# Optimization experiments

Measured on AMD Instinct MI355X. Metric: run time of the kernel, lower is better.

## Reference

```python
import jax, jax.numpy as jnp
import numpy as np

B, T = 64, 1024
VOCAB, EMBED, HIDDEN = 55, 64, 128


def setup_inputs() -> dict:
    key = jax.random.key(0)
    ks = jax.random.split(key, 15)
    stdv = 1.0 / np.sqrt(HIDDEN)
    u = lambda k, s: jax.random.uniform(k, s, jnp.float32, -stdv, stdv)
    return {
        "x": jax.random.randint(ks[0], (B, T), 0, VOCAB),
        "emb": jax.random.normal(ks[1], (VOCAB, EMBED), jnp.float32),
        "w_ih0": u(ks[2], (HIDDEN, EMBED)),
        "b_ih0": u(ks[3], (HIDDEN,)),
        "w_hh0": u(ks[4], (HIDDEN, HIDDEN)),
        "b_hh0": u(ks[5], (HIDDEN,)),
        "w_ih1": u(ks[6], (HIDDEN, HIDDEN)),
        "b_ih1": u(ks[7], (HIDDEN,)),
        "w_hh1": u(ks[8], (HIDDEN, HIDDEN)),
        "b_hh1": u(ks[9], (HIDDEN,)),
        "attn_w": u(ks[10], (HIDDEN, HIDDEN)),
        "attn_b": u(ks[11], (HIDDEN,)),
        "fc_w": u(ks[12], (VOCAB, 2 * HIDDEN)),
        "fc_b": u(ks[13], (VOCAB,)),
    }


def reference(x, emb, w_ih0, b_ih0, w_hh0, b_hh0, w_ih1, b_ih1, w_hh1, b_hh1,
              attn_w, attn_b, fc_w, fc_b):
    Bx, Tx = x.shape
    H = w_hh0.shape[0]
    e = emb[x]  # [B, T, E]

    def step(carry, x_t):  # x_t: [B, E]
        h0, h1 = carry
        h0 = jnp.tanh(x_t @ w_ih0.T + b_ih0 + h0 @ w_hh0.T + b_hh0)
        h1 = jnp.tanh(h0 @ w_ih1.T + b_ih1 + h1 @ w_hh1.T + b_hh1)
        return (h0, h1), h1

    init = (jnp.zeros((Bx, H), e.dtype), jnp.zeros((Bx, H), e.dtype))
    _, outs = jax.lax.scan(step, init, jnp.swapaxes(e, 0, 1))  # [T, B, H]
    outs = jnp.swapaxes(outs, 0, 1)  # [B, T, H]

    Q = outs @ attn_w.T + attn_b  # [B, T, H]
    scores = jnp.einsum('bth,bsh->bts', Q, outs) / jnp.sqrt(jnp.asarray(H, e.dtype))
    causal = jnp.tril(jnp.ones((Tx, Tx), bool))  # [T, T]
    scores = jnp.where(causal[None], scores, jnp.asarray(-jnp.inf, scores.dtype))
    attn = jax.nn.softmax(scores, axis=-1)
    context = jnp.einsum('bts,bsh->bth', attn, outs)  # [B, T, H]

    combined = jnp.concatenate([outs, context], axis=-1)  # [B, T, 2H]
    logits = combined @ fc_w.T + fc_b  # [B, T, vocab]
    return logits
```

## Files before the change

### kernel.cpp

```cpp
#include <hip/hip_runtime.h>
#include <hip/hip_bf16.h>
#include <cstdint>
#include <cstddef>


typedef __attribute__((ext_vector_type(8))) short short8;
typedef __attribute__((ext_vector_type(4))) float f32x4;

__device__ __forceinline__ float bf2f(unsigned short u) {
    union { unsigned int i; float f; } c; c.i = ((unsigned int)u) << 16; return c.f;
}
__device__ __forceinline__ unsigned short f2bf(float f) {
    union { float f; unsigned int i; } c; c.f = f;
    unsigned int u = c.i;
    u += 0x7fffu + ((u >> 16) & 1u);
    return (unsigned short)(u >> 16);
}
__device__ __forceinline__ unsigned int pk_bf16(float lo, float hi) {
    union { __hip_bfloat162 h2; unsigned int u; } c;
    c.h2 = __float22bfloat162_rn(make_float2(lo, hi));
    return c.u;
}
__device__ __forceinline__ float fast_tanh(float x) {
    float e = __expf(2.0f * x);
    return 1.0f - 2.0f * __builtin_amdgcn_rcpf(e + 1.0f);
}
__device__ __forceinline__ void bar_lds() {
    asm volatile("s_waitcnt lgkmcnt(0)\n\ts_barrier" ::: "memory");
}
__device__ __forceinline__ short8 ld_a_bf16(const float* p) {
    const float4* q = (const float4*)p;
    float4 f0 = q[0], f1 = q[1];
    short8 r;
    r[0]=(short)f2bf(f0.x); r[1]=(short)f2bf(f0.y);
    r[2]=(short)f2bf(f0.z); r[3]=(short)f2bf(f0.w);
    r[4]=(short)f2bf(f1.x); r[5]=(short)f2bf(f1.y);
    r[6]=(short)f2bf(f1.z); r[7]=(short)f2bf(f1.w);
    return r;
}
__device__ __forceinline__ void ld_fc_hilo(const float* p, short8& hi, short8& lo) {
    const float4* q = (const float4*)p;
    float4 f0 = q[0], f1 = q[1];
    float ff[8] = {f0.x, f0.y, f0.z, f0.w, f1.x, f1.y, f1.z, f1.w};
#pragma unroll
    for (int i = 0; i < 8; ++i) {
        unsigned short hb = f2bf(ff[i]);
        hi[i] = (short)hb;
        lo[i] = (short)f2bf(ff[i] - bf2f(hb));
    }
}
__device__ __forceinline__ void rel_store(int* p, int v) {
    __threadfence();
    __hip_atomic_store(p, v, __ATOMIC_RELEASE, __HIP_MEMORY_SCOPE_AGENT);
}
__device__ __forceinline__ int rlx_load(const int* p) {
    return __hip_atomic_load(p, __ATOMIC_RELAXED, __HIP_MEMORY_SCOPE_AGENT);
}
__device__ __forceinline__ void acq_touch(const int* p) {
    (void)__hip_atomic_load(p, __ATOMIC_ACQUIRE, __HIP_MEMORY_SCOPE_AGENT);
}

__global__ __launch_bounds__(128)
void k_we(const float* __restrict__ emb, const float* __restrict__ w_ih0,
          const float* __restrict__ b_ih0, const float* __restrict__ b_hh0,
          float* __restrict__ WE)
{
    __shared__ float ev[64];
    const int i = threadIdx.x;
    const int v = blockIdx.x;
    if (i < 64) ev[i] = emb[v * 64 + i];
    __syncthreads();
    float s = b_ih0[i] + b_hh0[i];
    const float* wr = w_ih0 + i * 64;
#pragma unroll
    for (int k = 0; k < 64; ++k) s += wr[k] * ev[k];
    WE[v * 128 + i] = s;
}

__global__ __launch_bounds__(256)
void k_weg(const int* __restrict__ x, const float* __restrict__ WE,
           float* __restrict__ WEg)
{
    __shared__ int xv[32];
    const int tid = threadIdx.x;
    const int b   = blockIdx.y;
    const int t0  = blockIdx.x * 32;
    if (tid < 32) xv[tid] = x[b * 1024 + t0 + tid];
    __syncthreads();
#pragma unroll
    for (int it = 0; it < 4; ++it) {
        int tt = it * 8 + (tid >> 5);
        int c4 = tid & 31;
        float4 v = ((const float4*)(WE + xv[tt] * 128))[c4];
        ((float4*)(WEg + ((size_t)b * 1024 + t0 + tt) * 128))[c4] = v;
    }
}

__global__ __launch_bounds__(1024)
void k_zero(int* __restrict__ f)
{
    f[threadIdx.x] = 0;
}

__global__ __launch_bounds__(512, 1)
void k_fused(const float* __restrict__ WEg,
             const float* __restrict__ w_hh0,
             const float* __restrict__ w_ih1, const float* __restrict__ b_ih1,
             const float* __restrict__ w_hh1, const float* __restrict__ b_hh1,
             unsigned short* __restrict__ outs_bf,
             unsigned short* __restrict__ outsT,
             const float* __restrict__ attn_w, const float* __restrict__ attn_b,
             const float* __restrict__ fc_w, const float* __restrict__ fc_b,
             float* __restrict__ out, int* __restrict__ flags)
{
    __shared__ __align__(16) unsigned char smem[100352];
    __shared__ int sidx;
    const int bx   = blockIdx.x;
    const int tid  = threadIdx.x;
    const int w    = tid >> 6;
    const int lane = tid & 63;
    const int quad = lane >> 4;
    const int n    = lane & 15;

    if (bx < 4) {
        typedef unsigned short (*HBuf)[16][136];
        HBuf h0buf = (HBuf)(smem);
        HBuf h1buf = (HBuf)(smem + 8704);
        const int bbase = bx * 16;

        if (w < 4) {
            const int r0 = w * 32 + quad * 4;
            const int r1 = r0 + 16;
            short8 a0[2][4];
#pragma unroll
            for (int r = 0; r < 2; ++r) {
                const size_t mrow = (size_t)(w * 32 + r * 16 + n) * 128;
#pragma unroll
                for (int ks = 0; ks < 4; ++ks)
                    a0[r][ks] = ld_a_bf16(w_hh0 + mrow + ks * 32 + quad * 8);
            }
            const size_t wegB0 = (size_t)(bbase + n) * 131072 + r0;
            const size_t wegB1 = wegB0 + 16;
            {
                float4 p0 = *(const float4*)(WEg + wegB0);
                float4 p1 = *(const float4*)(WEg + wegB1);
                *(uint2*)&h0buf[0][n][r0] = make_uint2(
                    pk_bf16(fast_tanh(p0.x), fast_tanh(p0.y)),
                    pk_bf16(fast_tanh(p0.z), fast_tanh(p0.w)));
                *(uint2*)&h0buf[0][n][r1] = make_uint2(
                    pk_bf16(fast_tanh(p1.x), fast_tanh(p1.y)),
                    pk_bf16(fast_tanh(p1.z), fast_tanh(p1.w)));
            }
            float4 wA0 = *(const float4*)(WEg + wegB0 + 128);
            float4 wA1 = *(const float4*)(WEg + wegB1 + 128);
            float4 wB0 = *(const float4*)(WEg + wegB0 + 256);
            float4 wB1 = *(const float4*)(WEg + wegB1 + 256);
            float4 wC0 = *(const float4*)(WEg + wegB0 + 384);
            float4 wC1 = *(const float4*)(WEg + wegB1 + 384);
            __syncthreads();

            for (int t = 0; t < 1024; ++t) {
                const int p = t & 1;
                if (t < 1023) {
                    const unsigned short* h0p = &h0buf[p][n][quad * 8];
                    short8 bh[4];
#pragma unroll
                    for (int ks = 0; ks < 4; ++ks)
                        bh[ks] = *(const short8*)(h0p + ks * 32);
                    f32x4 c0 = (f32x4){wA0.x, wA0.y, wA0.z, wA0.w};
                    f32x4 c1 = (f32x4){wA1.x, wA1.y, wA1.z, wA1.w};
#pragma unroll
                    for (int ks = 0; ks < 4; ++ks) {
                        c0 = __builtin_amdgcn_mfma_f32_16x16x32_bf16(a0[0][ks], bh[ks], c0, 0,0,0);
                        c1 = __builtin_amdgcn_mfma_f32_16x16x32_bf16(a0[1][ks], bh[ks], c1, 0,0,0);
                    }
                    wA0 = wB0; wA1 = wB1; wB0 = wC0; wB1 = wC1;
                    const size_t tpre = (size_t)((t + 4 < 1024) ? t + 4 : 1023) * 128;
                    wC0 = *(const float4*)(WEg + wegB0 + tpre);
                    wC1 = *(const float4*)(WEg + wegB1 + tpre);
                    *(uint2*)&h0buf[p ^ 1][n][r0] = make_uint2(
                        pk_bf16(fast_tanh(c0[0]), fast_tanh(c0[1])),
                        pk_bf16(fast_tanh(c0[2]), fast_tanh(c0[3])));
                    *(uint2*)&h0buf[p ^ 1][n][r1] = make_uint2(
                        pk_bf16(fast_tanh(c1[0]), fast_tanh(c1[1])),
                        pk_bf16(fast_tanh(c1[2]), fast_tanh(c1[3])));
                }
                bar_lds();
                if ((t & 127) == 127) {
                    asm volatile("s_waitcnt vmcnt(0)" ::: "memory");
                    __syncthreads();
                    if (tid == 0) rel_store(flags + bx, t + 1);
                }
            }
        } else {
            const int w2 = w - 4;
            const int r0 = w2 * 32 + quad * 4;
            const int r1 = r0 + 16;
            short8 a1[2][4], a2[2][4];
#pragma unroll
            for (int r = 0; r < 2; ++r) {
                const size_t mrow = (size_t)(w2 * 32 + r * 16 + n) * 128;
#pragma unroll
                for (int ks = 0; ks < 4; ++ks) {
                    a1[r][ks] = ld_a_bf16(w_ih1 + mrow + ks * 32 + quad * 8);
                    a2[r][ks] = ld_a_bf16(w_hh1 + mrow + ks * 32 + quad * 8);
                }
            }
            f32x4 b1i[2];
#pragma unroll
            for (int r = 0; r < 2; ++r)
#pragma unroll
                for (int j = 0; j < 4; ++j) {
                    int row = w2 * 32 + r * 16 + quad * 4 + j;
                    b1i[r][j] = b_ih1[row] + b_hh1[row];
                }
            *(uint2*)&h1buf[0][n][r0] = make_uint2(0u, 0u);
            *(uint2*)&h1buf[0][n][r1] = make_uint2(0u, 0u);
            unsigned short* outp0 = outs_bf + (size_t)(bbase + n) * 131072 + r0;
            unsigned short* outp1 = outp0 + 16;
            __syncthreads();

            for (int t = 0; t < 1024; ++t) {
                const int p = t & 1;
                const unsigned short* h0p = &h0buf[p][n][quad * 8];
                const unsigned short* h1p = &h1buf[p][n][quad * 8];
                short8 bh0[4], bh1[4];
#pragma unroll
                for (int ks = 0; ks < 4; ++ks) {
                    bh0[ks] = *(const short8*)(h0p + ks * 32);
                    bh1[ks] = *(const short8*)(h1p + ks * 32);
                }
                f32x4 c0 = b1i[0], c1 = b1i[1];
                f32x4 d0 = (f32x4){0.f,0.f,0.f,0.f}, d1 = (f32x4){0.f,0.f,0.f,0.f};
#pragma unroll
                for (int ks = 0; ks < 4; ++ks) {
                    c0 = __builtin_amdgcn_mfma_f32_16x16x32_bf16(a1[0][ks], bh0[ks], c0, 0,0,0);
                    c1 = __builtin_amdgcn_mfma_f32_16x16x32_bf16(a1[1][ks], bh0[ks], c1, 0,0,0);
                    d0 = __builtin_amdgcn_mfma_f32_16x16x32_bf16(a2[0][ks], bh1[ks], d0, 0,0,0);
                    d1 = __builtin_amdgcn_mfma_f32_16x16x32_bf16(a2[1][ks], bh1[ks], d1, 0,0,0);
                }
                uint2 o0 = make_uint2(
                    pk_bf16(fast_tanh(c0[0] + d0[0]), fast_tanh(c0[1] + d0[1])),
                    pk_bf16(fast_tanh(c0[2] + d0[2]), fast_tanh(c0[3] + d0[3])));
                uint2 o1 = make_uint2(
                    pk_bf16(fast_tanh(c1[0] + d1[0]), fast_tanh(c1[1] + d1[1])),
                    pk_bf16(fast_tanh(c1[2] + d1[2]), fast_tanh(c1[3] + d1[3])));
                *(uint2*)&h1buf[p ^ 1][n][r0] = o0;
                *(uint2*)&h1buf[p ^ 1][n][r1] = o1;
                *(uint2*)(outp0 + (size_t)t * 128) = o0;
                *(uint2*)(outp1 + (size_t)t * 128) = o1;
                bar_lds();
                if ((t & 127) == 127) {
                    asm volatile("s_waitcnt vmcnt(0)" ::: "memory");
                    __syncthreads();
                    if (tid == 0) rel_store(flags + bx, t + 1);
                }
            }
        }
        return;
    }

    int* qcnt = flags + 768;
    const float cscale = 0.08838834764831845f;

    for (;;) {
        __syncthreads();
        if (tid == 0) sidx = atomicAdd(qcnt, 1);
        __syncthreads();
        const int idx = sidx;
        if (idx >= 1024) break;
        const int group = idx >> 6;
        const int b     = idx & 63;
        const int c     = group >> 1;

        if (!(group & 1)) {
            if (tid == 0) {
                while (rlx_load(flags + (b >> 4)) < (c + 1) * 128)
                    __builtin_amdgcn_s_sleep(100);
            }
            __syncthreads();
            acq_touch(flags + (b >> 4));

            typedef unsigned short (*LT)[130];
            LT lt = (LT)smem;
            const int t0 = c * 128;
            const unsigned int* src =
                (const unsigned int*)(outs_bf + ((size_t)b * 1024 + t0) * 128);
            for (int i2 = tid; i2 < 8192; i2 += 512) {
                int tr = i2 >> 6, h2 = i2 & 63;
                unsigned int v = src[tr * 64 + h2];
                lt[tr][h2 * 2]     = (unsigned short)(v & 0xffffu);
                lt[tr][h2 * 2 + 1] = (unsigned short)(v >> 16);
            }
            __syncthreads();
            unsigned int* dst = (unsigned int*)(outsT + (size_t)b * 131072);
            for (int i2 = tid; i2 < 8192; i2 += 512) {
                int h = i2 >> 6, t2 = i2 & 63;
                unsigned int v = (unsigned int)lt[t2 * 2][h] |
                                 ((unsigned int)lt[t2 * 2 + 1][h] << 16);
                dst[h * 512 + (t0 >> 1) + t2] = v;
            }
            asm volatile("s_waitcnt vmcnt(0)" ::: "memory");
            __syncthreads();
            if (tid == 0) rel_store(flags + 16 + b * 8 + c, 1);
            continue;
        }

        {
            const int qt = c;
            if (tid == 0) {
                for (int cc = 0; cc <= qt; ++cc)
                    while (rlx_load(flags + 16 + b * 8 + cc) < 1)
                        __builtin_amdgcn_s_sleep(100);
            }
            __syncthreads();
            acq_touch(flags + 16 + b * 8 + qt);

            unsigned short* lK = (unsigned short*)smem;
            unsigned short* lV = (unsigned short*)(smem + 32768);
            unsigned short* lP = (unsigned short*)(smem + 65536);
            unsigned short* lPw = lP + w * 2176;

            const unsigned short* outsB = outs_bf + (size_t)b * 131072;
            const int qrow = qt * 128 + w * 16 + n;

            short8 bo[4];
#pragma unroll
            for (int ks = 0; ks < 4; ++ks)
                bo[ks] = *(const short8*)(outsB + (size_t)qrow * 128 + ks * 32 + quad * 8);
#pragma unroll
            for (int mt = 0; mt < 8; ++mt) {
                short8 aw[4];
#pragma unroll
                for (int ks = 0; ks < 4; ++ks)
                    aw[ks] = ld_a_bf16(attn_w + (size_t)(mt * 16 + n) * 128 + ks * 32 + quad * 8);
                f32x4 cq;
#pragma unroll
                for (int r = 0; r < 4; ++r) cq[r] = attn_b[mt * 16 + quad * 4 + r];
#pragma unroll
                for (int ks = 0; ks < 4; ++ks)
                    cq = __builtin_amdgcn_mfma_f32_16x16x32_bf16(aw[ks], bo[ks], cq, 0,0,0);
                *(uint2*)&lPw[n * 136 + mt * 16 + quad * 4] =
                    make_uint2(pk_bf16(cq[0], cq[1]), pk_bf16(cq[2], cq[3]));
            }
            short8 qf[4];
#pragma unroll
            for (int ks = 0; ks < 4; ++ks)
                qf[ks] = *(const short8*)&lPw[n * 136 + ks * 32 + quad * 8];

            f32x4 accO[8];
#pragma unroll
            for (int dt = 0; dt < 8; ++dt) accO[dt] = (f32x4){0.f, 0.f, 0.f, 0.f};
            float mx = -1e30f, lsum = 0.f;

            for (int kt = 0; kt <= qt; ++kt) {
                __syncthreads();
                for (int cc = tid; cc < 2048; cc += 512) {
                    int row = cc >> 4, k8 = cc & 15;
                    uint4 vk = *(const uint4*)(outsB + (size_t)(kt * 128 + row) * 128 + k8 * 8);
                    *(uint4*)&lK[row * 128 + ((k8 ^ (row & 15)) << 3)] = vk;
                    uint4 vv = *(const uint4*)(outsT + ((size_t)b * 128 + row) * 1024 +
                                               kt * 128 + k8 * 8);
                    *(uint4*)&lV[row * 128 + ((k8 ^ (row & 15)) << 3)] = vv;
                }
                __syncthreads();
                f32x4 accS[8];
#pragma unroll
                for (int mt = 0; mt < 8; ++mt) {
                    short8 af[4];
#pragma unroll
                    for (int ks = 0; ks < 4; ++ks) {
                        int r = mt * 16 + n;
                        af[ks] = *(const short8*)&lK[r * 128 + (((ks * 4 + quad) ^ (r & 15)) << 3)];
                    }
                    f32x4 s = (f32x4){0.f, 0.f, 0.f, 0.f};
#pragma unroll
                    for (int ks = 0; ks < 4; ++ks)
                        s = __builtin_amdgcn_mfma_f32_16x16x32_bf16(af[ks], qf[ks], s, 0,0,0);
                    accS[mt] = s;
                }
                if (kt == qt) {
                    const int ql = w * 16 + n;
#pragma unroll
                    for (int mt = 0; mt < 8; ++mt)
#pragma unroll
                        for (int jv = 0; jv < 4; ++jv)
                            if (mt * 16 + quad * 4 + jv > ql) accS[mt][jv] = -1e30f;
                }
                float tmax = accS[0][0];
#pragma unroll
                for (int mt = 0; mt < 8; ++mt)
#pragma unroll
                    for (int jv = 0; jv < 4; ++jv) tmax = fmaxf(tmax, accS[mt][jv]);
                tmax = fmaxf(tmax, __shfl_xor(tmax, 16));
                tmax = fmaxf(tmax, __shfl_xor(tmax, 32));
                float nm = fmaxf(mx, tmax);
                float alpha = __expf((mx - nm) * cscale);
                float ss = 0.f;
#pragma unroll
                for (int mt = 0; mt < 8; ++mt)
#pragma unroll
                    for (int jv = 0; jv < 4; ++jv) {
                        float p = __expf((accS[mt][jv] - nm) * cscale);
                        accS[mt][jv] = p;
                        ss += p;
                    }
                ss += __shfl_xor(ss, 16);
                ss += __shfl_xor(ss, 32);
                lsum = lsum * alpha + ss;
                mx = nm;
#pragma unroll
                for (int mt = 0; mt < 8; ++mt)
                    *(uint2*)&lPw[n * 136 + mt * 16 + quad * 4] = make_uint2(
                        pk_bf16(accS[mt][0], accS[mt][1]),
                        pk_bf16(accS[mt][2], accS[mt][3]));
#pragma unroll
                for (int dt = 0; dt < 8; ++dt)
#pragma unroll
                    for (int jv = 0; jv < 4; ++jv) accO[dt][jv] *= alpha;
                short8 pf[4];
#pragma unroll
                for (int ks = 0; ks < 4; ++ks)
                    pf[ks] = *(const short8*)&lPw[n * 136 + ks * 32 + quad * 8];
#pragma unroll
                for (int dt = 0; dt < 8; ++dt) {
                    short8 vf[4];
#pragma unroll
                    for (int ks = 0; ks < 4; ++ks) {
                        int d = dt * 16 + n;
                        vf[ks] = *(const short8*)&lV[d * 128 + (((ks * 4 + quad) ^ (d & 15)) << 3)];
                    }
#pragma unroll
                    for (int ks = 0; ks < 4; ++ks)
                        accO[dt] = __builtin_amdgcn_mfma_f32_16x16x32_bf16(vf[ks], pf[ks], accO[dt], 0,0,0);
                }
            }
            {
                float inv = __builtin_amdgcn_rcpf(lsum);
#pragma unroll
                for (int dt = 0; dt < 8; ++dt)
                    *(uint2*)&lPw[n * 136 + dt * 16 + quad * 4] = make_uint2(
                        pk_bf16(accO[dt][0] * inv, accO[dt][1] * inv),
                        pk_bf16(accO[dt][2] * inv, accO[dt][3] * inv));
            }
            short8 bC[4];
#pragma unroll
            for (int ks = 0; ks < 4; ++ks)
                bC[ks] = *(const short8*)&lPw[n * 136 + ks * 32 + quad * 8];
#pragma unroll
            for (int mt = 0; mt < 4; ++mt) {
                const int vrow = mt * 16 + n;
                f32x4 acc;
#pragma unroll
                for (int r = 0; r < 4; ++r) {
                    int vv = mt * 16 + quad * 4 + r;
                    acc[r] = (vv < 55) ? fc_b[vv] : 0.f;
                }
#pragma unroll
                for (int cc = 0; cc < 8; ++cc) {
                    short8 hi, lo;
                    if (vrow < 55) {
                        ld_fc_hilo(fc_w + (size_t)vrow * 256 + cc * 32 + quad * 8, hi, lo);
                    } else {
#pragma unroll
                        for (int ii = 0; ii < 8; ++ii) { hi[ii] = 0; lo[ii] = 0; }
                    }
                    short8 bb = (cc < 4) ? bo[cc] : bC[cc - 4];
                    acc = __builtin_amdgcn_mfma_f32_16x16x32_bf16(hi, bb, acc, 0,0,0);
                    acc = __builtin_amdgcn_mfma_f32_16x16x32_bf16(lo, bb, acc, 0,0,0);
                }
#pragma unroll
                for (int r = 0; r < 4; ++r) {
                    int vv = mt * 16 + quad * 4 + r;
                    if (vv < 55)
                        out[((size_t)b * 1024 + qrow) * 55 + vv] = acc[r];
                }
            }
        }
    }
}

extern "C" void kernel_launch(void* const* d_in, const int* in_sizes, int n_in,
                              void* d_out, int out_size, void* d_ws, size_t ws_size,
                              hipStream_t stream)
{
    const int*   x      = (const int*)d_in[0];
    const float* emb    = (const float*)d_in[1];
    const float* w_ih0  = (const float*)d_in[2];
    const float* b_ih0  = (const float*)d_in[3];
    const float* w_hh0  = (const float*)d_in[4];
    const float* b_hh0  = (const float*)d_in[5];
    const float* w_ih1  = (const float*)d_in[6];
    const float* b_ih1  = (const float*)d_in[7];
    const float* w_hh1  = (const float*)d_in[8];
    const float* b_hh1  = (const float*)d_in[9];
    const float* attn_w = (const float*)d_in[10];
    const float* attn_b = (const float*)d_in[11];
    const float* fc_w   = (const float*)d_in[12];
    const float* fc_b   = (const float*)d_in[13];
    float* out = (float*)d_out;

    char* ws = (char*)d_ws;
    unsigned short* outs_bf = (unsigned short*)(ws);
    unsigned short* outsT   = (unsigned short*)(ws + ((size_t)16 << 20));
    float*          WEp     = (float*)         (ws + ((size_t)32 << 20));
    int*            flags   = (int*)           (ws + ((size_t)32 << 20) + (64 << 10));
    float*          WEg     = (float*)         (ws + ((size_t)33 << 20));

    k_zero<<<dim3(1), dim3(1024), 0, stream>>>(flags);
    k_we<<<dim3(55), dim3(128), 0, stream>>>(emb, w_ih0, b_ih0, b_hh0, WEp);
    k_weg<<<dim3(32, 64), dim3(256), 0, stream>>>(x, WEp, WEg);
    k_fused<<<dim3(256), dim3(512), 0, stream>>>(
        WEg, w_hh0, w_ih1, b_ih1, w_hh1, b_hh1, outs_bf, outsT,
        attn_w, attn_b, fc_w, fc_b, out, flags);
}
```

Before: 846.2 us.

## Fuse embedding precompute into persistent kernel and split tail attention tiles

Moves the word-embedding projection and gather into the persistent fused kernel as work items, with flags so the recurrent blocks start as soon as their batch rows are gathered. This removes two separate kernel launches. The last two query tiles, which have the longest causal spans, are split across several work items that write partial softmax state to a workspace and are merged afterwards, shortening the serial tail. The cost is extra flag spin-waits, partial-result traffic and more complex scheduling, which adds deadlock risk if the work-queue order is wrong.

Result: slower. 874.5 us (+3.3%).

```diff
diff --git a/kernel.cpp b/kernel.cpp
--- a/kernel.cpp
+++ b/kernel.cpp
@@ -27,6 +27,9 @@
 }
 __device__ __forceinline__ void bar_lds() {
     asm volatile("s_waitcnt lgkmcnt(0)\n\ts_barrier" ::: "memory");
+}
+__device__ __forceinline__ void drain_vm() {
+    asm volatile("s_waitcnt vmcnt(0)" ::: "memory");
 }
 __device__ __forceinline__ short8 ld_a_bf16(const float* p) {
     const float4* q = (const float4*)p;
@@ -60,50 +63,18 @@
     (void)__hip_atomic_load(p, __ATOMIC_ACQUIRE, __HIP_MEMORY_SCOPE_AGENT);
 }
 
-__global__ __launch_bounds__(128)
-void k_we(const float* __restrict__ emb, const float* __restrict__ w_ih0,
-          const float* __restrict__ b_ih0, const float* __restrict__ b_hh0,
-          float* __restrict__ WE)
-{
-    __shared__ float ev[64];
-    const int i = threadIdx.x;
-    const int v = blockIdx.x;
-    if (i < 64) ev[i] = emb[v * 64 + i];
-    __syncthreads();
-    float s = b_ih0[i] + b_hh0[i];
-    const float* wr = w_ih0 + i * 64;
-#pragma unroll
-    for (int k = 0; k < 64; ++k) s += wr[k] * ev[k];
-    WE[v * 128 + i] = s;
-}
-
-__global__ __launch_bounds__(256)
-void k_weg(const int* __restrict__ x, const float* __restrict__ WE,
-           float* __restrict__ WEg)
-{
-    __shared__ int xv[32];
-    const int tid = threadIdx.x;
-    const int b   = blockIdx.y;
-    const int t0  = blockIdx.x * 32;
-    if (tid < 32) xv[tid] = x[b * 1024 + t0 + tid];
-    __syncthreads();
-#pragma unroll
-    for (int it = 0; it < 4; ++it) {
-        int tt = it * 8 + (tid >> 5);
-        int c4 = tid & 31;
-        float4 v = ((const float4*)(WE + xv[tt] * 128))[c4];
-        ((float4*)(WEg + ((size_t)b * 1024 + t0 + tt) * 128))[c4] = v;
-    }
-}
-
 __global__ __launch_bounds__(1024)
 void k_zero(int* __restrict__ f)
 {
     f[threadIdx.x] = 0;
+    f[threadIdx.x + 1024] = 0;
 }
 
 __global__ __launch_bounds__(512, 1)
-void k_fused(const float* __restrict__ WEg,
+void k_fused(const int* __restrict__ x, const float* __restrict__ emb,
+             const float* __restrict__ w_ih0, const float* __restrict__ b_ih0,
+             const float* __restrict__ b_hh0,
+             float* __restrict__ WEp, float* __restrict__ WEg,
              const float* __restrict__ w_hh0,
              const float* __restrict__ w_ih1, const float* __restrict__ b_ih1,
              const float* __restrict__ w_hh1, const float* __restrict__ b_hh1,
@@ -111,6 +82,7 @@
              unsigned short* __restrict__ outsT,
              const float* __restrict__ attn_w, const float* __restrict__ attn_b,
              const float* __restrict__ fc_w, const float* __restrict__ fc_b,
+             float* __restrict__ part_ws,
              float* __restrict__ out, int* __restrict__ flags)
 {
     __shared__ __align__(16) unsigned char smem[100352];
@@ -127,6 +99,14 @@
         HBuf h0buf = (HBuf)(smem);
         HBuf h1buf = (HBuf)(smem + 8704);
         const int bbase = bx * 16;
+
+        if (tid == 0) {
+            for (int i = 0; i < 16; ++i)
+                while (rlx_load(flags + 16 + bbase + i) < 1)
+                    __builtin_amdgcn_s_sleep(16);
+            acq_touch(flags);
+        }
+        __syncthreads();
 
         if (w < 4) {
             const int r0 = w * 32 + quad * 4;
@@ -187,7 +167,7 @@
                 }
                 bar_lds();
                 if ((t & 127) == 127) {
-                    asm volatile("s_waitcnt vmcnt(0)" ::: "memory");
+                    drain_vm();
                     __syncthreads();
                     if (tid == 0) rel_store(flags + bx, t + 1);
                 }
@@ -251,7 +231,7 @@
                 *(uint2*)(outp1 + (size_t)t * 128) = o1;
                 bar_lds();
                 if ((t & 127) == 127) {
-                    asm volatile("s_waitcnt vmcnt(0)" ::: "memory");
+                    drain_vm();
                     __syncthreads();
                     if (tid == 0) rel_store(flags + bx, t + 1);
                 }
@@ -260,7 +240,22 @@
         return;
     }
 
-    int* qcnt = flags + 768;
+    if (bx == 4) {
+        for (int o = tid; o < 7040; o += 512) {
+            int v = o >> 7, i = o & 127;
+            float s = b_ih0[i] + b_hh0[i];
+            const float* wr = w_ih0 + i * 64;
+            const float* ev = emb + v * 64;
+#pragma unroll 8
+            for (int k = 0; k < 64; ++k) s += wr[k] * ev[k];
+            WEp[v * 128 + i] = s;
+        }
+        drain_vm();
+        __syncthreads();
+        if (tid == 0) rel_store(flags + 8, 1);
+    }
+
+    int* qcnt = flags + 1100;
     const float cscale = 0.08838834764831845f;
 
     for (;;) {
@@ -268,22 +263,60 @@
         if (tid == 0) sidx = atomicAdd(qcnt, 1);
         __syncthreads();
         const int idx = sidx;
-        if (idx >= 1024) break;
-        const int group = idx >> 6;
-        const int b     = idx & 63;
-        const int c     = group >> 1;
-
-        if (!(group & 1)) {
+        if (idx >= 1280) break;
+
+        if (idx < 64) {
+            const int b = idx;
             if (tid == 0) {
-                while (rlx_load(flags + (b >> 4)) < (c + 1) * 128)
-                    __builtin_amdgcn_s_sleep(100);
-            }
-            __syncthreads();
-            acq_touch(flags + (b >> 4));
-
+                while (rlx_load(flags + 8) < 1) __builtin_amdgcn_s_sleep(16);
+                acq_touch(flags + 8);
+            }
+            __syncthreads();
+            for (int t0 = 0; t0 < 1024; t0 += 16) {
+                int tt = t0 + (tid >> 5), c4 = tid & 31;
+                int xv = x[b * 1024 + tt];
+                float4 v = ((const float4*)(WEp + xv * 128))[c4];
+                ((float4*)(WEg + ((size_t)b * 1024 + tt) * 128))[c4] = v;
+            }
+            drain_vm();
+            __syncthreads();
+            if (tid == 0) rel_store(flags + 16 + b, 1);
+            continue;
+        }
+
+        const int r = idx - 64;
+        int b, qt = 0, kt_lo = 0, kt_hi = 0, mode = 0;
+        int slot = 0, myflag = 0, npart = 0;
+        int pslot0 = 0, pflag0 = 0, pslot1 = 0, pflag1 = 0;
+        bool isT = false; int tc = 0;
+        if (r < 768) {
+            int c = r >> 7, sub = r & 127;
+            if (sub < 64) { isT = true; tc = c; b = sub; }
+            else { b = sub - 64; qt = c; mode = 0; kt_lo = 0; kt_hi = qt; }
+        } else if (r < 832) { isT = true; tc = 6; b = r - 768; }
+        else if (r < 896)  { b = r - 832; qt = 6; mode = 1; kt_lo = 0; kt_hi = 3;
+                             slot = b * 4 + 3; myflag = 960 + b; }
+        else if (r < 960)  { b = r - 896; qt = 6; mode = 2; kt_lo = 4; kt_hi = 6;
+                             npart = 1; pslot0 = b * 4 + 3; pflag0 = 960 + b; }
+        else if (r < 1024) { isT = true; tc = 7; b = r - 960; }
+        else if (r < 1088) { b = r - 1024; qt = 7; mode = 1; kt_lo = 0; kt_hi = 2;
+                             slot = b * 4 + 0; myflag = 768 + b * 2; }
+        else if (r < 1152) { b = r - 1088; qt = 7; mode = 1; kt_lo = 3; kt_hi = 5;
+                             slot = b * 4 + 1; myflag = 768 + b * 2 + 1; }
+        else               { b = r - 1152; qt = 7; mode = 2; kt_lo = 6; kt_hi = 7;
+                             npart = 2; pslot0 = b * 4 + 0; pflag0 = 768 + b * 2;
+                             pslot1 = b * 4 + 1; pflag1 = 768 + b * 2 + 1; }
+
+        if (isT) {
+            if (tid == 0) {
+                while (rlx_load(flags + (b >> 4)) < (tc + 1) * 128)
+                    __builtin_amdgcn_s_sleep(16);
+                acq_touch(flags);
+            }
+            __syncthreads();
             typedef unsigned short (*LT)[130];
             LT lt = (LT)smem;
-            const int t0 = c * 128;
+            const int t0 = tc * 128;
             const unsigned int* src =
                 (const unsigned int*)(outs_bf + ((size_t)b * 1024 + t0) * 128);
             for (int i2 = tid; i2 < 8192; i2 += 512) {
@@ -300,181 +333,227 @@
                                  ((unsigned int)lt[t2 * 2 + 1][h] << 16);
                 dst[h * 512 + (t0 >> 1) + t2] = v;
             }
-            asm volatile("s_waitcnt vmcnt(0)" ::: "memory");
-            __syncthreads();
-            if (tid == 0) rel_store(flags + 16 + b * 8 + c, 1);
+            drain_vm();
+            __syncthreads();
+            if (tid == 0) rel_store(flags + 192 + b * 8 + tc, 1);
             continue;
         }
 
+        if (tid == 0) {
+            while (rlx_load(flags + (b >> 4)) < (qt + 1) * 128)
+                __builtin_amdgcn_s_sleep(16);
+            for (int kk = kt_lo; kk <= kt_hi; ++kk)
+                while (rlx_load(flags + 192 + b * 8 + kk) < 1)
+                    __builtin_amdgcn_s_sleep(16);
+            acq_touch(flags);
+        }
+        __syncthreads();
+
+        unsigned short* lK = (unsigned short*)smem;
+        unsigned short* lV = (unsigned short*)(smem + 32768);
+        unsigned short* lP = (unsigned short*)(smem + 65536);
+        unsigned short* lPw = lP + w * 2176;
+
+        const unsigned short* outsB = outs_bf + (size_t)b * 131072;
+        const int qrow = qt * 128 + w * 16 + n;
+        const int q128 = w * 16 + n;
+
+        short8 bo[4];
+#pragma unroll
+        for (int ks = 0; ks < 4; ++ks)
+            bo[ks] = *(const short8*)(outsB + (size_t)qrow * 128 + ks * 32 + quad * 8);
+#pragma unroll
+        for (int mt = 0; mt < 8; ++mt) {
+            short8 aw[4];
+#pragma unroll
+            for (int ks = 0; ks < 4; ++ks)
+                aw[ks] = ld_a_bf16(attn_w + (size_t)(mt * 16 + n) * 128 + ks * 32 + quad * 8);
+            f32x4 cq;
+#pragma unroll
+            for (int rr = 0; rr < 4; ++rr) cq[rr] = attn_b[mt * 16 + quad * 4 + rr];
+#pragma unroll
+            for (int ks = 0; ks < 4; ++ks)
+                cq = __builtin_amdgcn_mfma_f32_16x16x32_bf16(aw[ks], bo[ks], cq, 0,0,0);
+            *(uint2*)&lPw[n * 136 + mt * 16 + quad * 4] =
+                make_uint2(pk_bf16(cq[0], cq[1]), pk_bf16(cq[2], cq[3]));
+        }
+        short8 qf[4];
+#pragma unroll
+        for (int ks = 0; ks < 4; ++ks)
+            qf[ks] = *(const short8*)&lPw[n * 136 + ks * 32 + quad * 8];
+
+        f32x4 accO[8];
+#pragma unroll
+        for (int dt = 0; dt < 8; ++dt) accO[dt] = (f32x4){0.f, 0.f, 0.f, 0.f};
+        float mx = -1e30f, lsum = 0.f;
+
+        for (int kt = kt_lo; kt <= kt_hi; ++kt) {
+            __syncthreads();
+            for (int cc = tid; cc < 2048; cc += 512) {
+                int row = cc >> 4, k8 = cc & 15;
+                uint4 vk = *(const uint4*)(outsB + (size_t)(kt * 128 + row) * 128 + k8 * 8);
+                *(uint4*)&lK[row * 128 + ((k8 ^ (row & 15)) << 3)] = vk;
+                uint4 vv = *(const uint4*)(outsT + ((size_t)b * 128 + row) * 1024 +
+                                           kt * 128 + k8 * 8);
+                *(uint4*)&lV[row * 128 + ((k8 ^ (row & 15)) << 3)] = vv;
+            }
+            __syncthreads();
+            f32x4 accS[8];
+#pragma unroll
+            for (int mt = 0; mt < 8; ++mt) {
+                short8 af[4];
+#pragma unroll
+                for (int ks = 0; ks < 4; ++ks) {
+                    int rr = mt * 16 + n;
+                    af[ks] = *(const short8*)&lK[rr * 128 + (((ks * 4 + quad) ^ (rr & 15)) << 3)];
+                }
+                f32x4 s = (f32x4){0.f, 0.f, 0.f, 0.f};
+#pragma unroll
+                for (int ks = 0; ks < 4; ++ks)
+                    s = __builtin_amdgcn_mfma_f32_16x16x32_bf16(af[ks], qf[ks], s, 0,0,0);
+                accS[mt] = s;
+            }
+            if (kt == qt) {
+#pragma unroll
+                for (int mt = 0; mt < 8; ++mt)
+#pragma unroll
+                    for (int jv = 0; jv < 4; ++jv)
+                        if (mt * 16 + quad * 4 + jv > q128) accS[mt][jv] = -1e30f;
+            }
+            float tmax = accS[0][0];
+#pragma unroll
+            for (int mt = 0; mt < 8; ++mt)
+#pragma unroll
+                for (int jv = 0; jv < 4; ++jv) tmax = fmaxf(tmax, accS[mt][jv]);
+            tmax = fmaxf(tmax, __shfl_xor(tmax, 16));
+            tmax = fmaxf(tmax, __shfl_xor(tmax, 32));
+            float nm = fmaxf(mx, tmax);
+            float alpha = __expf((mx - nm) * cscale);
+            float ss = 0.f;
+#pragma unroll
+            for (int mt = 0; mt < 8; ++mt)
+#pragma unroll
+                for (int jv = 0; jv < 4; ++jv) {
+                    float p = __expf((accS[mt][jv] - nm) * cscale);
+                    accS[mt][jv] = p;
+                    ss += p;
+                }
+            ss += __shfl_xor(ss, 16);
+            ss += __shfl_xor(ss, 32);
+            lsum = lsum * alpha + ss;
+            mx = nm;
+#pragma unroll
+            for (int mt = 0; mt < 8; ++mt)
+                *(uint2*)&lPw[n * 136 + mt * 16 + quad * 4] = make_uint2(
+                    pk_bf16(accS[mt][0], accS[mt][1]),
+                    pk_bf16(accS[mt][2], accS[mt][3]));
+#pragma unroll
+            for (int dt = 0; dt < 8; ++dt)
+#pragma unroll
+                for (int jv = 0; jv < 4; ++jv) accO[dt][jv] *= alpha;
+            short8 pf[4];
+#pragma unroll
+            for (int ks = 0; ks < 4; ++ks)
+                pf[ks] = *(const short8*)&lPw[n * 136 + ks * 32 + quad * 8];
+#pragma unroll
+            for (int dt = 0; dt < 8; ++dt) {
+                short8 vf[4];
+#pragma unroll
+                for (int ks = 0; ks < 4; ++ks) {
+                    int d = dt * 16 + n;
+                    vf[ks] = *(const short8*)&lV[d * 128 + (((ks * 4 + quad) ^ (d & 15)) << 3)];
+                }
+#pragma unroll
+                for (int ks = 0; ks < 4; ++ks)
+                    accO[dt] = __builtin_amdgcn_mfma_f32_16x16x32_bf16(vf[ks], pf[ks], accO[dt], 0,0,0);
+            }
+        }
+
+        if (mode == 1) {
+            float* wsO = part_ws + (size_t)slot * 17408;
+            float4* po = (float4*)wsO;
+#pragma unroll
+            for (int dt = 0; dt < 8; ++dt)
+                po[(w * 64 + lane) * 8 + dt] =
+                    make_float4(accO[dt][0], accO[dt][1], accO[dt][2], accO[dt][3]);
+            if (quad == 0) {
+                wsO[16384 + q128 * 2]     = mx;
+                wsO[16384 + q128 * 2 + 1] = lsum;
+            }
+            drain_vm();
+            __syncthreads();
+            if (tid == 0) rel_store(flags + myflag, 1);
+            continue;
+        }
+
+        if (mode == 2) {
+            for (int p = 0; p < npart; ++p) {
+                const int ps = (p == 0) ? pslot0 : pslot1;
+                const int pfl = (p == 0) ? pflag0 : pflag1;
+                if (tid == 0) {
+                    while (rlx_load(flags + pfl) < 1) __builtin_amdgcn_s_sleep(16);
+                    acq_touch(flags + pfl);
+                }
+                __syncthreads();
+                const float* wsO = part_ws + (size_t)ps * 17408;
+                const float4* po = (const float4*)wsO;
+                float m0 = wsO[16384 + q128 * 2];
+                float l0 = wsO[16384 + q128 * 2 + 1];
+                float nm = fmaxf(mx, m0);
+                float a1 = __expf((mx - nm) * cscale);
+                float a0 = __expf((m0 - nm) * cscale);
+#pragma unroll
+                for (int dt = 0; dt < 8; ++dt) {
+                    float4 p4 = po[(w * 64 + lane) * 8 + dt];
+                    accO[dt][0] = accO[dt][0] * a1 + p4.x * a0;
+                    accO[dt][1] = accO[dt][1] * a1 + p4.y * a0;
+                    accO[dt][2] = accO[dt][2] * a1 + p4.z * a0;
+                    accO[dt][3] = accO[dt][3] * a1 + p4.w * a0;
+                }
+                lsum = lsum * a1 + l0 * a0;
+                mx = nm;
+            }
+        }
+
         {
-            const int qt = c;
-            if (tid == 0) {
-                for (int cc = 0; cc <= qt; ++cc)
-                    while (rlx_load(flags + 16 + b * 8 + cc) < 1)
-                        __builtin_amdgcn_s_sleep(100);
-            }
-            __syncthreads();
-            acq_touch(flags + 16 + b * 8 + qt);
-
-            unsigned short* lK = (unsigned short*)smem;
-            unsigned short* lV = (unsigned short*)(smem + 32768);
-            unsigned short* lP = (unsigned short*)(smem + 65536);
-            unsigned short* lPw = lP + w * 2176;
-
-            const unsigned short* outsB = outs_bf + (size_t)b * 131072;
-            const int qrow = qt * 128 + w * 16 + n;
-
-            short8 bo[4];
-#pragma unroll
-            for (int ks = 0; ks < 4; ++ks)
-                bo[ks] = *(const short8*)(outsB + (size_t)qrow * 128 + ks * 32 + quad * 8);
-#pragma unroll
-            for (int mt = 0; mt < 8; ++mt) {
-                short8 aw[4];
-#pragma unroll
-                for (int ks = 0; ks < 4; ++ks)
-                    aw[ks] = ld_a_bf16(attn_w + (size_t)(mt * 16 + n) * 128 + ks * 32 + quad * 8);
-                f32x4 cq;
-#pragma unroll
-                for (int r = 0; r < 4; ++r) cq[r] = attn_b[mt * 16 + quad * 4 + r];
-#pragma unroll
-                for (int ks = 0; ks < 4; ++ks)
-                    cq = __builtin_amdgcn_mfma_f32_16x16x32_bf16(aw[ks], bo[ks], cq, 0,0,0);
-                *(uint2*)&lPw[n * 136 + mt * 16 + quad * 4] =
-                    make_uint2(pk_bf16(cq[0], cq[1]), pk_bf16(cq[2], cq[3]));
-            }
-            short8 qf[4];
-#pragma unroll
-            for (int ks = 0; ks < 4; ++ks)
-                qf[ks] = *(const short8*)&lPw[n * 136 + ks * 32 + quad * 8];
-
-            f32x4 accO[8];
-#pragma unroll
-            for (int dt = 0; dt < 8; ++dt) accO[dt] = (f32x4){0.f, 0.f, 0.f, 0.f};
-            float mx = -1e30f, lsum = 0.f;
-
-            for (int kt = 0; kt <= qt; ++kt) {
-                __syncthreads();
-                for (int cc = tid; cc < 2048; cc += 512) {
-                    int row = cc >> 4, k8 = cc & 15;
-                    uint4 vk = *(const uint4*)(outsB + (size_t)(kt * 128 + row) * 128 + k8 * 8);
-                    *(uint4*)&lK[row * 128 + ((k8 ^ (row & 15)) << 3)] = vk;
-                    uint4 vv = *(const uint4*)(outsT + ((size_t)b * 128 + row) * 1024 +
-                                               kt * 128 + k8 * 8);
-                    *(uint4*)&lV[row * 128 + ((k8 ^ (row & 15)) << 3)] = vv;
-                }
-                __syncthreads();
-                f32x4 accS[8];
-#pragma unroll
-                for (int mt = 0; mt < 8; ++mt) {
-                    short8 af[4];
-#pragma unroll
-                    for (int ks = 0; ks < 4; ++ks) {
-                        int r = mt * 16 + n;
-                        af[ks] = *(const short8*)&lK[r * 128 + (((ks * 4 + quad) ^ (r & 15)) << 3)];
-                    }
-                    f32x4 s = (f32x4){0.f, 0.f, 0.f, 0.f};
-#pragma unroll
-                    for (int ks = 0; ks < 4; ++ks)
-                        s = __builtin_amdgcn_mfma_f32_16x16x32_bf16(af[ks], qf[ks], s, 0,0,0);
-                    accS[mt] = s;
-                }
-                if (kt == qt) {
-                    const int ql = w * 16 + n;
-#pragma unroll
-                    for (int mt = 0; mt < 8; ++mt)
-#pragma unroll
-                        for (int jv = 0; jv < 4; ++jv)
-                            if (mt * 16 + quad * 4 + jv > ql) accS[mt][jv] = -1e30f;
-                }
-                float tmax = accS[0][0];
-#pragma unroll
-                for (int mt = 0; mt < 8; ++mt)
-#pragma unroll
-                    for (int jv = 0; jv < 4; ++jv) tmax = fmaxf(tmax, accS[mt][jv]);
-                tmax = fmaxf(tmax, __shfl_xor(tmax, 16));
-                tmax = fmaxf(tmax, __shfl_xor(tmax, 32));
-                float nm = fmaxf(mx, tmax);
-                float alpha = __expf((mx - nm) * cscale);
-                float ss = 0.f;
-#pragma unroll
-                for (int mt = 0; mt < 8; ++mt)
-#pragma unroll
-                    for (int jv = 0; jv < 4; ++jv) {
-                        float p = __expf((accS[mt][jv] - nm) * cscale);
-                        accS[mt][jv] = p;
-                        ss += p;
-                    }
-                ss += __shfl_xor(ss, 16);
-                ss += __shfl_xor(ss, 32);
-                lsum = lsum * alpha + ss;
-                mx = nm;
-#pragma unroll
-                for (int mt = 0; mt < 8; ++mt)
-                    *(uint2*)&lPw[n * 136 + mt * 16 + quad * 4] = make_uint2(
-                        pk_bf16(accS[mt][0], accS[mt][1]),
-                        pk_bf16(accS[mt][2], accS[mt][3]));
-#pragma unroll
-                for (int dt = 0; dt < 8; ++dt)
-#pragma unroll
-                    for (int jv = 0; jv < 4; ++jv) accO[dt][jv] *= alpha;
-                short8 pf[4];
-#pragma unroll
-                for (int ks = 0; ks < 4; ++ks)
-                    pf[ks] = *(const short8*)&lPw[n * 136 + ks * 32 + quad * 8];
-#pragma unroll
-                for (int dt = 0; dt < 8; ++dt) {
-                    short8 vf[4];
-#pragma unroll
-                    for (int ks = 0; ks < 4; ++ks) {
-                        int d = dt * 16 + n;
-                        vf[ks] = *(const short8*)&lV[d * 128 + (((ks * 4 + quad) ^ (d & 15)) << 3)];
-                    }
-#pragma unroll
-                    for (int ks = 0; ks < 4; ++ks)
-                        accO[dt] = __builtin_amdgcn_mfma_f32_16x16x32_bf16(vf[ks], pf[ks], accO[dt], 0,0,0);
-                }
-            }
-            {
-                float inv = __builtin_amdgcn_rcpf(lsum);
-#pragma unroll
-                for (int dt = 0; dt < 8; ++dt)
-                    *(uint2*)&lPw[n * 136 + dt * 16 + quad * 4] = make_uint2(
-                        pk_bf16(accO[dt][0] * inv, accO[dt][1] * inv),
-                        pk_bf16(accO[dt][2] * inv, accO[dt][3] * inv));
-            }
-            short8 bC[4];
-#pragma unroll
-            for (int ks = 0; ks < 4; ++ks)
-                bC[ks] = *(const short8*)&lPw[n * 136 + ks * 32 + quad * 8];
-#pragma unroll
-            for (int mt = 0; mt < 4; ++mt) {
-                const int vrow = mt * 16 + n;
-                f32x4 acc;
-#pragma unroll
-                for (int r = 0; r < 4; ++r) {
-                    int vv = mt * 16 + quad * 4 + r;
-                    acc[r] = (vv < 55) ? fc_b[vv] : 0.f;
-                }
-#pragma unroll
-                for (int cc = 0; cc < 8; ++cc) {
-                    short8 hi, lo;
-                    if (vrow < 55) {
-                        ld_fc_hilo(fc_w + (size_t)vrow * 256 + cc * 32 + quad * 8, hi, lo);
-                    } else {
-#pragma unroll
-                        for (int ii = 0; ii < 8; ++ii) { hi[ii] = 0; lo[ii] = 0; }
-                    }
-                    short8 bb = (cc < 4) ? bo[cc] : bC[cc - 4];
-                    acc = __builtin_amdgcn_mfma_f32_16x16x32_bf16(hi, bb, acc, 0,0,0);
-                    acc = __builtin_amdgcn_mfma_f32_16x16x32_bf16(lo, bb, acc, 0,0,0);
-                }
-#pragma unroll
-                for (int r = 0; r < 4; ++r) {
-                    int vv = mt * 16 + quad * 4 + r;
-                    if (vv < 55)
-                        out[((size_t)b * 1024 + qrow) * 55 + vv] = acc[r];
-                }
+            float inv = __builtin_amdgcn_rcpf(lsum);
+#pragma unroll
+            for (int dt = 0; dt < 8; ++dt)
+                *(uint2*)&lPw[n * 136 + dt * 16 + quad * 4] = make_uint2(
+                    pk_bf16(accO[dt][0] * inv, accO[dt][1] * inv),
+                    pk_bf16(accO[dt][2] * inv, accO[dt][3] * inv));
+        }
+        short8 bC[4];
+#pragma unroll
+        for (int ks = 0; ks < 4; ++ks)
+            bC[ks] = *(const short8*)&lPw[n * 136 + ks * 32 + quad * 8];
+#pragma unroll
+        for (int mt = 0; mt < 4; ++mt) {
+            const int vrow = mt * 16 + n;
+            f32x4 acc;
+#pragma unroll
+            for (int rr = 0; rr < 4; ++rr) {
+                int vv = mt * 16 + quad * 4 + rr;
+                acc[rr] = (vv < 55) ? fc_b[vv] : 0.f;
+            }
+#pragma unroll
+            for (int cc = 0; cc < 8; ++cc) {
+                short8 hi, lo;
+                if (vrow < 55) {
+                    ld_fc_hilo(fc_w + (size_t)vrow * 256 + cc * 32 + quad * 8, hi, lo);
+                } else {
+#pragma unroll
+                    for (int ii = 0; ii < 8; ++ii) { hi[ii] = 0; lo[ii] = 0; }
+                }
+                short8 bb = (cc < 4) ? bo[cc] : bC[cc - 4];
+                acc = __builtin_amdgcn_mfma_f32_16x16x32_bf16(hi, bb, acc, 0,0,0);
+                acc = __builtin_amdgcn_mfma_f32_16x16x32_bf16(lo, bb, acc, 0,0,0);
+            }
+#pragma unroll
+            for (int rr = 0; rr < 4; ++rr) {
+                int vv = mt * 16 + quad * 4 + rr;
+                if (vv < 55)
+                    out[((size_t)b * 1024 + qrow) * 55 + vv] = acc[rr];
             }
         }
     }
@@ -506,11 +585,11 @@
     float*          WEp     = (float*)         (ws + ((size_t)32 << 20));
     int*            flags   = (int*)           (ws + ((size_t)32 << 20) + (64 << 10));
     float*          WEg     = (float*)         (ws + ((size_t)33 << 20));
+    float*          part_ws = (float*)         (ws + ((size_t)66 << 20));
 
     k_zero<<<dim3(1), dim3(1024), 0, stream>>>(flags);
-    k_we<<<dim3(55), dim3(128), 0, stream>>>(emb, w_ih0, b_ih0, b_hh0, WEp);
-    k_weg<<<dim3(32, 64), dim3(256), 0, stream>>>(x, WEp, WEg);
     k_fused<<<dim3(256), dim3(512), 0, stream>>>(
-        WEg, w_hh0, w_ih1, b_ih1, w_hh1, b_hh1, outs_bf, outsT,
-        attn_w, attn_b, fc_w, fc_b, out, flags);
-}
+        x, emb, w_ih0, b_ih0, b_hh0, WEp, WEg,
+        w_hh0, w_ih1, b_ih1, w_hh1, b_hh1, outs_bf, outsT,
+        attn_w, attn_b, fc_w, fc_b, part_ws, out, flags);
+}
```
